# Kernel tuning notes

Hardware: AMD Instinct MI355X
Metric: run time of the kernel (lower is better)

The kernel has to match this reference:

```python
import jax, jax.numpy as jnp
import numpy as np

B, C, N = 8, 3, 4096
NSAMPLE = 10
MLP = (64, 64)
# checkerboard re-gather pattern from the original module
INDS = np.array([0, 1, 2, 3, 2, 3, 4, 5, 4, 5, 6, 7, 6, 7, 8, 9])


def setup_inputs() -> dict:
    key = jax.random.key(0)
    k1, k2, k3 = jax.random.split(key, 3)
    pos = jax.random.normal(k1, (B, C, N), jnp.float32)
    w1 = jax.random.normal(k2, (MLP[0], 4 * C, 2, 2), jnp.float32) * 0.1  # Conv2d(12, mlp0, k=2)
    b1 = jnp.zeros((MLP[0],), jnp.float32)
    w2 = jax.random.normal(k3, (MLP[1], MLP[0]), jnp.float32) * 0.1       # Conv2d(mlp0, mlp1, k=1)
    b2 = jnp.zeros((MLP[1],), jnp.float32)
    return {"pos": pos, "w1": w1, "b1": b1, "w2": w2, "b2": b2}


def _squeeze_2x2_alt(x):
    # x: [B, N, c, 4, 4] -> [B, N, 4c, 2, 2] with channel order [a, d, b, c]
    a = x[..., 0::2, 0::2]  # (0,0) of each 2x2 block
    d = x[..., 1::2, 1::2]  # (1,1)
    b = x[..., 0::2, 1::2]  # (0,1)
    c = x[..., 1::2, 0::2]  # (1,0)
    return jnp.concatenate([a, d, b, c], axis=-3)


def reference(pos, w1, b1, w2, b2):
    Bn, Cn, Nn = pos.shape
    pos_t = pos.transpose(0, 2, 1)  # [B, N, C]
    # pairwise squared distances [B, N, N]
    sq = jnp.sum(pos_t * pos_t, axis=-1)
    d2 = sq[:, :, None] - 2.0 * jnp.einsum('bnc,bmc->bnm', pos_t, pos_t) + sq[:, None, :]
    _, idx = jax.lax.top_k(-d2, NSAMPLE)  # [B, N, K] nearest neighbors (self first)
    # grouping_operation: grouped[b,c,n,k] = pos[b,c,idx[b,n,k]]
    grouped = jax.vmap(lambda p, i: p[:, i])(pos, idx)  # [B, C, N, K]
    pg = grouped[..., INDS]                              # [B, C, N, 16]
    pg = pg.transpose(0, 2, 1, 3).reshape(Bn, Nn, Cn, 4, 4)  # [B, N, 3, 4, 4]
    sqz = _squeeze_2x2_alt(pg)                           # [B, N, 12, 2, 2]
    # Conv2d(12->mlp0, k=2, stride=1) over 2x2 spatial == full contraction
    h = jnp.einsum('bnchw,ochw->bno', sqz, w1) + b1      # [B, N, mlp0]
    out = jnp.einsum('bno,po->bnp', h, w2) + b2          # [B, N, mlp1]
    return out.transpose(0, 2, 1)                        # [B, mlp1, N]
```

## Files before the change

### kernel.cpp

```cpp
#include <hip/hip_runtime.h>
#include <math.h>

#define NPTS 4096
#define NSMP 10

typedef float f32x2 __attribute__((ext_vector_type(2)));

__global__ __launch_bounds__(256) void prep_kernel(
    const float* __restrict__ w1, const float* __restrict__ b1,
    const float* __restrict__ w2, const float* __restrict__ b2,
    float* __restrict__ wn, float* __restrict__ bb) {
  __shared__ float w1l[64 * 48];
  __shared__ float w2t[64 * 64];
  __shared__ float b1l[64];
  __shared__ float part[4][30][64];
  __shared__ float bpart[4][64];
  const int t = threadIdx.x, p = t & 63, grp = t >> 6, o0 = grp * 16;
  for (int idx = t; idx < 64 * 48; idx += 256) w1l[idx] = w1[idx];
  for (int idx = t; idx < 64 * 64; idx += 256) w2t[(idx & 63) * 64 + (idx >> 6)] = w2[idx];
  if (t < 64) b1l[t] = b1[t];
  __syncthreads();

  const int sg[16] = {0,2,4,6, 3,5,7,9, 1,3,5,7, 2,4,6,8};
  float w2r[16];
  #pragma unroll
  for (int oo = 0; oo < 16; ++oo) w2r[oo] = w2t[(o0 + oo) * 64 + p];
  float wloc[30];
  #pragma unroll
  for (int i = 0; i < 30; ++i) wloc[i] = 0.0f;
  #pragma unroll
  for (int g = 0; g < 4; ++g)
    #pragma unroll
    for (int i = 0; i < 2; ++i)
      #pragma unroll
      for (int j = 0; j < 2; ++j) {
        const int s = sg[g * 4 + i * 2 + j];
        #pragma unroll
        for (int c = 0; c < 3; ++c) {
          const int k = (c + 3 * g) * 4 + i * 2 + j;
          float wk = 0.0f;
          #pragma unroll
          for (int oo = 0; oo < 16; ++oo)
            wk = fmaf(w2r[oo], w1l[(o0 + oo) * 48 + k], wk);
          wloc[s * 3 + c] += wk;
        }
      }
  #pragma unroll
  for (int i = 0; i < 30; ++i) part[grp][i][p] = wloc[i];
  float sb = 0.0f;
  #pragma unroll
  for (int oo = 0; oo < 16; ++oo) sb = fmaf(w2r[oo], b1l[o0 + oo], sb);
  bpart[grp][p] = sb;
  __syncthreads();
  const float* p0 = &part[0][0][0];
  for (int idx = t; idx < 30 * 64; idx += 256)
    wn[idx] = p0[idx] + p0[1920 + idx] + p0[3840 + idx] + p0[5760 + idx];
  if (t < 64) bb[t] = b2[t] + bpart[0][t] + bpart[1][t] + bpart[2][t] + bpart[3][t];
}

__global__ __launch_bounds__(1024, 4) void topk_kernel(const float* __restrict__ pos,
                                                       int* __restrict__ idx_out) {
  __shared__ float4 pts[NPTS];
  __shared__ int cnt[16][8];
  __shared__ int bufi[16][8][64];

  const int b = blockIdx.y, tid = threadIdx.x, lane = tid & 63, wv = tid >> 6;
  const float* pb = pos + (size_t)b * 3 * NPTS;
  for (int i = tid; i < NPTS; i += 1024) {
    float x = pb[i], y = pb[i + NPTS], z = pb[i + 2 * NPTS];
    float sq = __fadd_rn(__fadd_rn(__fmul_rn(x, x), __fmul_rn(y, y)), __fmul_rn(z, z));
    pts[i] = make_float4(x, y, z, sq);
  }
  __syncthreads();

  const int n0 = blockIdx.x * 128 + wv * 8;

  f32x2 qx[4], qy[4], qz[4], dmin[4];
  #pragma unroll
  for (int pp = 0; pp < 4; ++pp) {
    float4 qa = pts[n0 + 2 * pp], qb = pts[n0 + 2 * pp + 1];
    qx[pp].x = qa.x; qx[pp].y = qb.x;
    qy[pp].x = qa.y; qy[pp].y = qb.y;
    qz[pp].x = qa.z; qz[pp].y = qb.z;
    dmin[pp].x = INFINITY; dmin[pp].y = INFINITY;
  }

  #pragma unroll 8
  for (int k = 0; k < 64; ++k) {
    float4 p = pts[k * 64 + lane];
    #pragma unroll
    for (int pp = 0; pp < 4; ++pp) {
      f32x2 dot = qx[pp] * p.x + qy[pp] * p.y + qz[pp] * p.z;
      f32x2 key = (-2.0f) * dot + p.w;
      dmin[pp] = __builtin_elementwise_min(dmin[pp], key);
    }
  }

  unsigned um[8], lo[8], hi[8];
  #pragma unroll
  for (int r = 0; r < 8; ++r) {
    float dm = (r & 1) ? dmin[r >> 1].y : dmin[r >> 1].x;
    unsigned ub = __float_as_uint(dm);
    um[r] = (ub & 0x80000000u) ? ~ub : (ub | 0x80000000u);
    lo[r] = 0u; hi[r] = 0xFFFFFFFFu;
  }
  #pragma unroll 1
  for (int it = 0; it < 24; ++it) {
    #pragma unroll
    for (int r = 0; r < 8; ++r) {
      unsigned mid = lo[r] + ((hi[r] - lo[r]) >> 1);
      int c10 = __popcll(__ballot(um[r] <= mid));
      if (c10 >= NSMP) hi[r] = mid; else lo[r] = mid + 1;
    }
  }
  float tx[8];
  #pragma unroll
  for (int r = 0; r < 8; ++r) {
    unsigned tb = (hi[r] & 0x80000000u) ? (hi[r] ^ 0x80000000u) : ~hi[r];
    float tf = __uint_as_float(tb);
    tx[r] = __fadd_rn(__fadd_rn(tf, 2e-4f), __fmul_rn(fabsf(tf), 1e-5f));
  }

  if (lane < 8) cnt[wv][lane] = 0;

  #pragma unroll 4
  for (int k = 0; k < 64; ++k) {
    float4 p = pts[k * 64 + lane];
    #pragma unroll
    for (int pp = 0; pp < 4; ++pp) {
      f32x2 dot = qx[pp] * p.x + qy[pp] * p.y + qz[pp] * p.z;
      f32x2 key = (-2.0f) * dot + p.w;
      if (key.x <= tx[2 * pp]) {
        int ps = atomicAdd(&cnt[wv][2 * pp], 1);
        if (ps < 64) bufi[wv][2 * pp][ps] = k * 64 + lane;
      }
      if (key.y <= tx[2 * pp + 1]) {
        int ps = atomicAdd(&cnt[wv][2 * pp + 1], 1);
        if (ps < 64) bufi[wv][2 * pp + 1][ps] = k * 64 + lane;
      }
    }
  }

  int c[8], si[8], rank[8];
  double dd[8];
  int cmax = 0;
  #pragma unroll
  for (int r = 0; r < 8; ++r) {
    c[r] = __builtin_amdgcn_readfirstlane(cnt[wv][r]);
    if (c[r] > 64) c[r] = 64;
    cmax = (c[r] > cmax) ? c[r] : cmax;
    rank[r] = 0;
  }
  #pragma unroll
  for (int r = 0; r < 8; ++r) {
    float qxr = (r & 1) ? qx[r >> 1].y : qx[r >> 1].x;
    float qyr = (r & 1) ? qy[r >> 1].y : qy[r >> 1].x;
    float qzr = (r & 1) ? qz[r >> 1].y : qz[r >> 1].x;
    if (lane < c[r]) {
      si[r] = bufi[wv][r][lane];
      float4 p = pts[si[r]];
      double dqx = (double)qxr, dqy = (double)qyr, dqz = (double)qzr;
      double px = (double)p.x, py = (double)p.y, pz = (double)p.z;
      double dot = dqx * px + dqy * py + dqz * pz;
      double sqn = dqx * dqx + dqy * dqy + dqz * dqz;
      double sqm = px * px + py * py + pz * pz;
      dd[r] = (sqn - 2.0 * dot) + sqm;
    } else { dd[r] = (double)INFINITY; si[r] = 0x7FFFFFFF; }
  }
  #pragma unroll 1
  for (int j = 0; j < cmax; ++j) {
    #pragma unroll
    for (int r = 0; r < 8; ++r) {
      int jlo = __builtin_amdgcn_readlane(__double2loint(dd[r]), j);
      int jhi = __builtin_amdgcn_readlane(__double2hiint(dd[r]), j);
      int ji  = __builtin_amdgcn_readlane(si[r], j);
      double jd = __hiloint2double(jhi, jlo);
      if (jd < dd[r] || (jd == dd[r] && ji < si[r])) ++rank[r];
    }
  }
  #pragma unroll
  for (int r = 0; r < 8; ++r)
    if (lane < c[r] && rank[r] < NSMP)
      idx_out[((size_t)b * NPTS + n0 + r) * NSMP + rank[r]] = si[r];
}

__global__ __launch_bounds__(128) void mlp_kernel(const float* __restrict__ pos,
                                                  const int* __restrict__ nbr,
                                                  const float* __restrict__ wn,
                                                  const float* __restrict__ bbg,
                                                  float* __restrict__ out) {
  __shared__ __align__(16) float wl[30 * 64];
  __shared__ float bl[64];
  const int b = blockIdx.y;
  const int tid = threadIdx.x;
  for (int i = tid; i < 30 * 64; i += 128) wl[i] = wn[i];
  if (tid < 64) bl[tid] = bbg[tid];
  __syncthreads();

  const int n = blockIdx.x * 128 + tid;
  const float* pb = pos + (size_t)b * 3 * NPTS;
  const int* ip = nbr + ((size_t)b * NPTS + n) * NSMP;

  float pxyz[30];
  #pragma unroll
  for (int s = 0; s < NSMP; ++s) {
    int i = ip[s];
    pxyz[s * 3 + 0] = pb[i];
    pxyz[s * 3 + 1] = pb[i + NPTS];
    pxyz[s * 3 + 2] = pb[i + 2 * NPTS];
  }

  float acc[64];
  #pragma unroll
  for (int p = 0; p < 64; ++p) acc[p] = bl[p];
  #pragma unroll
  for (int sc = 0; sc < 30; ++sc) {
    float vv = pxyz[sc];
    const float4* w4 = (const float4*)(&wl[sc * 64]);
    #pragma unroll
    for (int pq = 0; pq < 16; ++pq) {
      float4 w = w4[pq];
      acc[pq * 4 + 0] = fmaf(w.x, vv, acc[pq * 4 + 0]);
      acc[pq * 4 + 1] = fmaf(w.y, vv, acc[pq * 4 + 1]);
      acc[pq * 4 + 2] = fmaf(w.z, vv, acc[pq * 4 + 2]);
      acc[pq * 4 + 3] = fmaf(w.w, vv, acc[pq * 4 + 3]);
    }
  }

  float* ob = out + ((size_t)b * 64) * NPTS + n;
  #pragma unroll
  for (int p = 0; p < 64; ++p) ob[p * NPTS] = acc[p];
}

extern "C" void kernel_launch(void* const* d_in, const int* in_sizes, int n_in,
                              void* d_out, int out_size, void* d_ws, size_t ws_size,
                              hipStream_t stream) {
  (void)in_sizes; (void)n_in; (void)out_size; (void)ws_size;
  const float* pos = (const float*)d_in[0];
  const float* w1  = (const float*)d_in[1];
  const float* b1  = (const float*)d_in[2];
  const float* w2  = (const float*)d_in[3];
  const float* b2  = (const float*)d_in[4];
  float* out = (float*)d_out;

  int*   nbr = (int*)d_ws;
  float* wn  = (float*)((char*)d_ws + 1310720);
  float* bb  = (float*)((char*)d_ws + 1310720 + 30 * 64 * 4);

  prep_kernel<<<dim3(1), dim3(256), 0, stream>>>(w1, b1, w2, b2, wn, bb);
  topk_kernel<<<dim3(32, 8), dim3(1024), 0, stream>>>(pos, nbr);
  mlp_kernel<<<dim3(32, 8), dim3(128), 0, stream>>>(pos, nbr, wn, bb, out);
}
```

Before: 150.3 us.

## Fuse neighbor MLP into top-k kernel and fold -2 scale into queries

Removes the separate MLP kernel: each wave keeps its 8 query neighbor lists in shared memory, gathers neighbor coordinates from the shared point cache, and computes all 64 output channels (one per lane) with register-held folded weights, writing float4 rows. Pre-scales query coordinates by -2 so the distance key uses three FMAs, and trims the binary-search threshold iterations from 24 to 20. This removes the global neighbor-index round trip and one launch, at the cost of extra registers in an already heavy kernel and a coarser threshold that may admit more candidates.

```diff
diff --git a/kernel.cpp b/kernel.cpp
--- a/kernel.cpp
+++ b/kernel.cpp
@@ -59,10 +59,13 @@
 }
 
 __global__ __launch_bounds__(1024, 4) void topk_kernel(const float* __restrict__ pos,
-                                                       int* __restrict__ idx_out) {
+                                                       const float* __restrict__ wng,
+                                                       const float* __restrict__ bbg,
+                                                       float* __restrict__ out) {
   __shared__ float4 pts[NPTS];
   __shared__ int cnt[16][8];
   __shared__ int bufi[16][8][64];
+  __shared__ int nbrL[16][8][NSMP];
 
   const int b = blockIdx.y, tid = threadIdx.x, lane = tid & 63, wv = tid >> 6;
   const float* pb = pos + (size_t)b * 3 * NPTS;
@@ -71,17 +74,21 @@
     float sq = __fadd_rn(__fadd_rn(__fmul_rn(x, x), __fmul_rn(y, y)), __fmul_rn(z, z));
     pts[i] = make_float4(x, y, z, sq);
   }
+  float wnr[30];
+  #pragma unroll
+  for (int sc = 0; sc < 30; ++sc) wnr[sc] = wng[sc * 64 + lane];
+  const float blv = bbg[lane];
   __syncthreads();
 
   const int n0 = blockIdx.x * 128 + wv * 8;
 
-  f32x2 qx[4], qy[4], qz[4], dmin[4];
+  f32x2 qx2[4], qy2[4], qz2[4], dmin[4];
   #pragma unroll
   for (int pp = 0; pp < 4; ++pp) {
     float4 qa = pts[n0 + 2 * pp], qb = pts[n0 + 2 * pp + 1];
-    qx[pp].x = qa.x; qx[pp].y = qb.x;
-    qy[pp].x = qa.y; qy[pp].y = qb.y;
-    qz[pp].x = qa.z; qz[pp].y = qb.z;
+    qx2[pp].x = -2.0f * qa.x; qx2[pp].y = -2.0f * qb.x;
+    qy2[pp].x = -2.0f * qa.y; qy2[pp].y = -2.0f * qb.y;
+    qz2[pp].x = -2.0f * qa.z; qz2[pp].y = -2.0f * qb.z;
     dmin[pp].x = INFINITY; dmin[pp].y = INFINITY;
   }
 
@@ -90,8 +97,9 @@
     float4 p = pts[k * 64 + lane];
     #pragma unroll
     for (int pp = 0; pp < 4; ++pp) {
-      f32x2 dot = qx[pp] * p.x + qy[pp] * p.y + qz[pp] * p.z;
-      f32x2 key = (-2.0f) * dot + p.w;
+      f32x2 key = qx2[pp] * p.x + p.w;
+      key = qy2[pp] * p.y + key;
+      key = qz2[pp] * p.z + key;
       dmin[pp] = __builtin_elementwise_min(dmin[pp], key);
     }
   }
@@ -105,7 +113,7 @@
     lo[r] = 0u; hi[r] = 0xFFFFFFFFu;
   }
   #pragma unroll 1
-  for (int it = 0; it < 24; ++it) {
+  for (int it = 0; it < 20; ++it) {
     #pragma unroll
     for (int r = 0; r < 8; ++r) {
       unsigned mid = lo[r] + ((hi[r] - lo[r]) >> 1);
@@ -128,8 +136,9 @@
     float4 p = pts[k * 64 + lane];
     #pragma unroll
     for (int pp = 0; pp < 4; ++pp) {
-      f32x2 dot = qx[pp] * p.x + qy[pp] * p.y + qz[pp] * p.z;
-      f32x2 key = (-2.0f) * dot + p.w;
+      f32x2 key = qx2[pp] * p.x + p.w;
+      key = qy2[pp] * p.y + key;
+      key = qz2[pp] * p.z + key;
       if (key.x <= tx[2 * pp]) {
         int ps = atomicAdd(&cnt[wv][2 * pp], 1);
         if (ps < 64) bufi[wv][2 * pp][ps] = k * 64 + lane;
@@ -153,13 +162,11 @@
   }
   #pragma unroll
   for (int r = 0; r < 8; ++r) {
-    float qxr = (r & 1) ? qx[r >> 1].y : qx[r >> 1].x;
-    float qyr = (r & 1) ? qy[r >> 1].y : qy[r >> 1].x;
-    float qzr = (r & 1) ? qz[r >> 1].y : qz[r >> 1].x;
+    float4 qa = pts[n0 + r];
     if (lane < c[r]) {
       si[r] = bufi[wv][r][lane];
       float4 p = pts[si[r]];
-      double dqx = (double)qxr, dqy = (double)qyr, dqz = (double)qzr;
+      double dqx = (double)qa.x, dqy = (double)qa.y, dqz = (double)qa.z;
       double px = (double)p.x, py = (double)p.y, pz = (double)p.z;
       double dot = dqx * px + dqy * py + dqz * pz;
       double sqn = dqx * dqx + dqy * dqy + dqz * dqz;
@@ -181,55 +188,29 @@
   #pragma unroll
   for (int r = 0; r < 8; ++r)
     if (lane < c[r] && rank[r] < NSMP)
-      idx_out[((size_t)b * NPTS + n0 + r) * NSMP + rank[r]] = si[r];
-}
-
-__global__ __launch_bounds__(128) void mlp_kernel(const float* __restrict__ pos,
-                                                  const int* __restrict__ nbr,
-                                                  const float* __restrict__ wn,
-                                                  const float* __restrict__ bbg,
-                                                  float* __restrict__ out) {
-  __shared__ __align__(16) float wl[30 * 64];
-  __shared__ float bl[64];
-  const int b = blockIdx.y;
-  const int tid = threadIdx.x;
-  for (int i = tid; i < 30 * 64; i += 128) wl[i] = wn[i];
-  if (tid < 64) bl[tid] = bbg[tid];
-  __syncthreads();
-
-  const int n = blockIdx.x * 128 + tid;
-  const float* pb = pos + (size_t)b * 3 * NPTS;
-  const int* ip = nbr + ((size_t)b * NPTS + n) * NSMP;
-
-  float pxyz[30];
-  #pragma unroll
-  for (int s = 0; s < NSMP; ++s) {
-    int i = ip[s];
-    pxyz[s * 3 + 0] = pb[i];
-    pxyz[s * 3 + 1] = pb[i + NPTS];
-    pxyz[s * 3 + 2] = pb[i + 2 * NPTS];
-  }
-
-  float acc[64];
-  #pragma unroll
-  for (int p = 0; p < 64; ++p) acc[p] = bl[p];
-  #pragma unroll
-  for (int sc = 0; sc < 30; ++sc) {
-    float vv = pxyz[sc];
-    const float4* w4 = (const float4*)(&wl[sc * 64]);
-    #pragma unroll
-    for (int pq = 0; pq < 16; ++pq) {
-      float4 w = w4[pq];
-      acc[pq * 4 + 0] = fmaf(w.x, vv, acc[pq * 4 + 0]);
-      acc[pq * 4 + 1] = fmaf(w.y, vv, acc[pq * 4 + 1]);
-      acc[pq * 4 + 2] = fmaf(w.z, vv, acc[pq * 4 + 2]);
-      acc[pq * 4 + 3] = fmaf(w.w, vv, acc[pq * 4 + 3]);
-    }
-  }
-
-  float* ob = out + ((size_t)b * 64) * NPTS + n;
-  #pragma unroll
-  for (int p = 0; p < 64; ++p) ob[p * NPTS] = acc[p];
+      nbrL[wv][r][rank[r]] = si[r];
+
+  float acc[8];
+  #pragma unroll
+  for (int r = 0; r < 8; ++r) acc[r] = blv;
+  #pragma unroll 1
+  for (int r = 0; r < 8; ++r) {
+    float a = acc[r];
+    #pragma unroll
+    for (int s = 0; s < NSMP; ++s) {
+      int id = nbrL[wv][r][s];
+      float4 pv = pts[id];
+      a = fmaf(wnr[s * 3 + 0], pv.x, a);
+      a = fmaf(wnr[s * 3 + 1], pv.y, a);
+      a = fmaf(wnr[s * 3 + 2], pv.z, a);
+    }
+    acc[r] = a;
+  }
+  float* ob = out + ((size_t)b * 64 + lane) * NPTS + n0;
+  float4 v0 = make_float4(acc[0], acc[1], acc[2], acc[3]);
+  float4 v1 = make_float4(acc[4], acc[5], acc[6], acc[7]);
+  *(float4*)(ob)     = v0;
+  *(float4*)(ob + 4) = v1;
 }
 
 extern "C" void kernel_launch(void* const* d_in, const int* in_sizes, int n_in,
@@ -243,11 +224,9 @@
   const float* b2  = (const float*)d_in[4];
   float* out = (float*)d_out;
 
-  int*   nbr = (int*)d_ws;
-  float* wn  = (float*)((char*)d_ws + 1310720);
-  float* bb  = (float*)((char*)d_ws + 1310720 + 30 * 64 * 4);
+  float* wn = (float*)d_ws;
+  float* bb = (float*)((char*)d_ws + 30 * 64 * 4);
 
   prep_kernel<<<dim3(1), dim3(256), 0, stream>>>(w1, b1, w2, b2, wn, bb);
-  topk_kernel<<<dim3(32, 8), dim3(1024), 0, stream>>>(pos, nbr);
-  mlp_kernel<<<dim3(32, 8), dim3(128), 0, stream>>>(pos, nbr, wn, bb, out);
+  topk_kernel<<<dim3(32, 8), dim3(1024), 0, stream>>>(pos, wn, bb, out);
 }
```

Measured after the change: 135.7 us. 9.7% less time.
